# Performance work log

Hardware: AMD Instinct MI355X
Metric: run time of the kernel (lower is better)

## Reference

```python
import jax, jax.numpy as jnp
import numpy as np

HEADS = 16
DIM_HEAD = 64
QUERY_DIM = 1024
INNER = HEADS * DIM_HEAD


def setup_inputs() -> dict:
    key = jax.random.key(0)
    ks = jax.random.split(key, 6)
    b, n = 4, 2048
    s = 0.02
    return {
        "x": jax.random.normal(ks[0], (b, n, QUERY_DIM), dtype=jnp.float32),
        "Wq": jax.random.normal(ks[1], (QUERY_DIM, INNER), dtype=jnp.float32) * s,
        "Wk": jax.random.normal(ks[2], (QUERY_DIM, INNER), dtype=jnp.float32) * s,
        "Wv": jax.random.normal(ks[3], (QUERY_DIM, INNER), dtype=jnp.float32) * s,
        "Wo": jax.random.normal(ks[4], (INNER, QUERY_DIM), dtype=jnp.float32) * s,
        "bo": jax.random.normal(ks[5], (QUERY_DIM,), dtype=jnp.float32) * s,
    }


def reference(x, Wq, Wk, Wv, Wo, bo):
    b, n, _ = x.shape
    scale = DIM_HEAD ** (-0.5)
    # project and split heads: [b, n, inner] -> [b, h, n, d]
    def split(t):
        return t.reshape(b, n, HEADS, DIM_HEAD).transpose(0, 2, 1, 3)
    q = split(x @ Wq)
    k = split(x @ Wk)
    v = split(x @ Wv)
    sim = jnp.einsum('bhid,bhjd->bhij', q, k) * scale  # [b, h, n, n]
    attn = jax.nn.softmax(sim, axis=-1)
    out = jnp.einsum('bhij,bhjd->bhid', attn, v)  # [b, h, n, d]
    out = out.transpose(0, 2, 1, 3).reshape(b, n, INNER)
    return out @ Wo + bo
```

## Files before the change

### kernel.cpp

```cpp
#include <hip/hip_runtime.h>

typedef __attribute__((ext_vector_type(8))) short bf16x8;
typedef __attribute__((ext_vector_type(4))) float f32x4;
typedef __attribute__((ext_vector_type(16))) float f32x16;
typedef __attribute__((ext_vector_type(2))) unsigned u32x2;

__device__ __forceinline__ unsigned short f2b(float f) {
  union { float f; unsigned u; } x; x.f = f;
  unsigned r = x.u + 0x7fffu + ((x.u >> 16) & 1u);
  return (unsigned short)(r >> 16);
}

__device__ __forceinline__ int cvt_pk_bf16(float lo, float hi) {
  int r;
  asm("v_cvt_pk_bf16_f32 %0, %1, %2" : "=v"(r) : "v"(lo), "v"(hi));
  return r;
}

__device__ __forceinline__ float exp2_fast(float x) {
#if __has_builtin(__builtin_amdgcn_exp2f)
  return __builtin_amdgcn_exp2f(x);
#else
  return __expf(x * 0.69314718055994531f);
#endif
}

__device__ __forceinline__ void gl_lds16(const unsigned short* g, unsigned short* l) {
  __builtin_amdgcn_global_load_lds(
      (const __attribute__((address_space(1))) unsigned int*)(unsigned long long)g,
      (__attribute__((address_space(3))) unsigned int*)(unsigned)(unsigned long long)l,
      16, 0, 0);
}

#define MFMA(a, b, c) __builtin_amdgcn_mfma_f32_16x16x32_bf16((a), (b), (c), 0, 0, 0)
#define MFMA32(a, b, c) __builtin_amdgcn_mfma_f32_32x32x16_bf16((a), (b), (c), 0, 0, 0)

__global__ __launch_bounds__(256) void convert_x(const float* __restrict__ x,
                                                 unsigned short* __restrict__ xb) {
  int i = (blockIdx.x * 256 + threadIdx.x) * 4;
  float4 v = *(const float4*)(x + i);
  ushort4 o;
  o.x = f2b(v.x); o.y = f2b(v.y); o.z = f2b(v.z); o.w = f2b(v.w);
  *(ushort4*)(xb + i) = o;
}

__global__ __launch_bounds__(256) void transpose_w(const float* __restrict__ wq, const float* __restrict__ wk,
                                                   const float* __restrict__ wv, const float* __restrict__ wo,
                                                   unsigned short* __restrict__ tq, unsigned short* __restrict__ tk,
                                                   unsigned short* __restrict__ tv, unsigned short* __restrict__ to_) {
  int z = blockIdx.z;
  const float* W = (z == 0) ? wq : (z == 1) ? wk : (z == 2) ? wv : wo;
  unsigned short* T = (z == 0) ? tq : (z == 1) ? tk : (z == 2) ? tv : to_;
  float scale = (z == 0) ? 0.125f * 1.4426950408889634f : 1.0f;
  __shared__ float tile[64][65];
  int tr = blockIdx.y * 64, tc = blockIdx.x * 64;
  int t = threadIdx.x;
  int col = t & 63, r0 = (t >> 6) * 16;
#pragma unroll
  for (int r = 0; r < 16; r++)
    tile[r0 + r][col] = W[(long)(tr + r0 + r) * 1024 + tc + col];
  __syncthreads();
  int k = t & 63, n0 = (t >> 6) * 16;
#pragma unroll
  for (int n = 0; n < 16; n++)
    T[(long)(tc + n0 + n) * 1024 + tr + k] = f2b(tile[k][n0 + n] * scale);
}

__device__ __forceinline__ void gemm_tile_128(const unsigned short* __restrict__ A,
                                              const unsigned short* __restrict__ BT,
                                              int m0, int n0, f32x4 acc[4][4],
                                              unsigned short* As, unsigned short* Bs,
                                              int lane, int wid) {
  const int wr = wid >> 1, wc = wid & 1;
  const int c = lane & 15, g = lane >> 4;
  for (int kt = 0; kt < 32; kt++) {
    __syncthreads();
#pragma unroll
    for (int ii = 0; ii < 2; ii++) {
      int chunk = (wid * 2 + ii) * 64 + lane;
      int row = chunk >> 2, rc = chunk & 3;
      gl_lds16(A + (long)(m0 + row) * 1024 + kt * 32 + rc * 8, As + (wid * 2 + ii) * 512);
      gl_lds16(BT + (long)(n0 + row) * 1024 + kt * 32 + rc * 8, Bs + (wid * 2 + ii) * 512);
    }
    __syncthreads();
    bf16x8 af[4], bfr[4];
#pragma unroll
    for (int mi = 0; mi < 4; mi++)
      af[mi] = *(const bf16x8*)(As + (wr * 64 + mi * 16 + c) * 32 + g * 8);
#pragma unroll
    for (int ni = 0; ni < 4; ni++)
      bfr[ni] = *(const bf16x8*)(Bs + (wc * 64 + ni * 16 + c) * 32 + g * 8);
#pragma unroll
    for (int mi = 0; mi < 4; mi++)
#pragma unroll
      for (int ni = 0; ni < 4; ni++)
        acc[mi][ni] = MFMA(af[mi], bfr[ni], acc[mi][ni]);
  }
}

__global__ __launch_bounds__(256) void gemm_qkv(const unsigned short* __restrict__ xb,
                                                const unsigned short* __restrict__ wtq,
                                                const unsigned short* __restrict__ wtk,
                                                const unsigned short* __restrict__ wtv,
                                                unsigned short* __restrict__ Qw,
                                                unsigned short* __restrict__ Kw,
                                                unsigned short* __restrict__ Vtw) {
  __shared__ unsigned short As[128 * 32], Bs[128 * 32];
  int m0 = blockIdx.x * 128;
  int nglob = blockIdx.y * 128;
  int which = nglob >> 10;
  const unsigned short* BT = (which == 0) ? wtq : (which == 1) ? wtk : wtv;
  int n0 = nglob & 1023;
  int lane = threadIdx.x & 63, wid = threadIdx.x >> 6;
  f32x4 acc[4][4] = {};
  gemm_tile_128(xb, BT, m0, n0, acc, As, Bs, lane, wid);

  const int wr = wid >> 1, wc = wid & 1;
  const int c = lane & 15, g = lane >> 4;
  int b = m0 >> 11;
  int ibase = (m0 & 2047);
#pragma unroll
  for (int mi = 0; mi < 4; mi++) {
    int irow0 = ibase + wr * 64 + mi * 16 + g * 4;
#pragma unroll
    for (int ni = 0; ni < 4; ni++) {
      int nl = n0 + wc * 64 + ni * 16 + c;
      int h = nl >> 6, d = nl & 63;
      if (which == 2) {
        ushort4 pk;
        pk.x = f2b(acc[mi][ni][0]); pk.y = f2b(acc[mi][ni][1]);
        pk.z = f2b(acc[mi][ni][2]); pk.w = f2b(acc[mi][ni][3]);
        *(ushort4*)(Vtw + ((long)(b * 16 + h) * 64 + d) * 2048 + irow0) = pk;
      } else {
        unsigned short* dst = (which == 0) ? Qw : Kw;
#pragma unroll
        for (int r = 0; r < 4; r++)
          dst[((long)(b * 16 + h) * 2048 + irow0 + r) * 64 + d] = f2b(acc[mi][ni][r]);
      }
    }
  }
}

__global__ __launch_bounds__(512) void attn(const unsigned short* __restrict__ Qw,
                                            const unsigned short* __restrict__ Kw,
                                            const unsigned short* __restrict__ Vtw,
                                            unsigned short* __restrict__ Ow) {
  int ib = blockIdx.y * 8 + blockIdx.x;
  int xcd = ib & 7, j = ib >> 3;
  int bh = xcd * 8 + (j >> 3);
  int qt = j & 7;
  int t = threadIdx.x;
  int lane = t & 63, wid = t >> 6;
  int c5 = lane & 31, h = lane >> 5;
  __shared__ unsigned short Ks[2][64 * 64];
  __shared__ unsigned short Vs[2][64 * 64];

  const unsigned short* Qp = Qw + ((long)bh * 2048 + qt * 256 + wid * 32 + c5) * 64 + h * 8;
  bf16x8 qf[4];
#pragma unroll
  for (int dK = 0; dK < 4; dK++) qf[dK] = *(const bf16x8*)(Qp + dK * 16);

  f32x16 oacc0 = {}, oacc1 = {};
  float ls0 = 0.f, ls1 = 0.f, ls2 = 0.f, ls3 = 0.f;

  const unsigned short* Kbase = Kw + (long)bh * 2048 * 64;
  const unsigned short* Vbase = Vtw + (long)bh * 64 * 2048;

#define STAGE(jt_, buf_)                                                              \
  {                                                                                   \
    int row = t >> 3, ch = t & 7;                                                     \
    int sw = ch ^ (row & 7);                                                          \
    gl_lds16(Kbase + (long)((jt_) * 64 + row) * 64 + sw * 8, &Ks[buf_][t * 8]);       \
    gl_lds16(Vbase + (long)row * 2048 + (jt_) * 64 + sw * 8, &Vs[buf_][t * 8]);       \
  }

  STAGE(0, 0);

  union FR { int i[4]; bf16x8 v; };

  for (int jt = 0; jt < 32; jt++) {
    int buf = jt & 1;
    __syncthreads();
    if (jt + 1 < 32) STAGE(jt + 1, buf ^ 1);

    f32x16 s0 = {}, s1 = {};
#pragma unroll
    for (int dK = 0; dK < 4; dK++) {
      int sw = ((dK * 2 + h) ^ (c5 & 7)) * 8;
      bf16x8 k0 = *(const bf16x8*)(&Ks[buf][c5 * 64 + sw]);
      bf16x8 k1 = *(const bf16x8*)(&Ks[buf][c5 * 64 + sw + 2048]);
      s0 = MFMA32(k0, qf[dK], s0);
      s1 = MFMA32(k1, qf[dK], s1);
    }

    int pk[2][4][2];
#pragma unroll
    for (int q2 = 0; q2 < 4; q2++) {
      float a0 = exp2_fast(s0[q2 * 4 + 0]), a1 = exp2_fast(s0[q2 * 4 + 1]);
      float a2 = exp2_fast(s0[q2 * 4 + 2]), a3 = exp2_fast(s0[q2 * 4 + 3]);
      ls0 += a0 + a1; ls1 += a2 + a3;
      pk[0][q2][0] = cvt_pk_bf16(a0, a1);
      pk[0][q2][1] = cvt_pk_bf16(a2, a3);
      float b0 = exp2_fast(s1[q2 * 4 + 0]), b1 = exp2_fast(s1[q2 * 4 + 1]);
      float b2 = exp2_fast(s1[q2 * 4 + 2]), b3 = exp2_fast(s1[q2 * 4 + 3]);
      ls2 += b0 + b1; ls3 += b2 + b3;
      pk[1][q2][0] = cvt_pk_bf16(b0, b1);
      pk[1][q2][1] = cvt_pk_bf16(b2, b3);
    }

#pragma unroll
    for (int kblk = 0; kblk < 4; kblk++) {
      int kvb = kblk >> 1, e2c = (kblk & 1) * 2;
      u32x2 p0 = __builtin_amdgcn_permlane32_swap((unsigned)pk[kvb][e2c][0],
                                                  (unsigned)pk[kvb][e2c + 1][0], false, false);
      u32x2 p1 = __builtin_amdgcn_permlane32_swap((unsigned)pk[kvb][e2c][1],
                                                  (unsigned)pk[kvb][e2c + 1][1], false, false);
      FR fr;
      fr.i[0] = (int)p0[0];
      fr.i[1] = (int)p1[0];
      fr.i[2] = (int)p0[1];
      fr.i[3] = (int)p1[1];
      int sw = ((kblk * 2 + h) ^ (c5 & 7)) * 8;
      bf16x8 v0 = *(const bf16x8*)(&Vs[buf][c5 * 64 + sw]);
      bf16x8 v1 = *(const bf16x8*)(&Vs[buf][c5 * 64 + sw + 2048]);
      oacc0 = MFMA32(v0, fr.v, oacc0);
      oacc1 = MFMA32(v1, fr.v, oacc1);
    }
  }
#undef STAGE

  float lsum = ls0 + ls1 + ls2 + ls3;
  lsum += __shfl_xor(lsum, 32);
  float inv = 1.0f / lsum;
  int b = bh >> 4, hh = bh & 15;
  long row = (long)b * 2048 + qt * 256 + wid * 32 + c5;
  unsigned short* orow = Ow + row * 1024 + hh * 64;
#pragma unroll
  for (int dblk = 0; dblk < 2; dblk++) {
#pragma unroll
    for (int q2 = 0; q2 < 4; q2++) {
      float o0 = (dblk ? oacc1 : oacc0)[q2 * 4 + 0] * inv;
      float o1 = (dblk ? oacc1 : oacc0)[q2 * 4 + 1] * inv;
      float o2 = (dblk ? oacc1 : oacc0)[q2 * 4 + 2] * inv;
      float o3 = (dblk ? oacc1 : oacc0)[q2 * 4 + 3] * inv;
      ushort4 pkv;
      pkv.x = f2b(o0); pkv.y = f2b(o1); pkv.z = f2b(o2); pkv.w = f2b(o3);
      *(ushort4*)(orow + dblk * 32 + q2 * 8 + h * 4) = pkv;
    }
  }
}

__global__ __launch_bounds__(256) void gemm_out(const unsigned short* __restrict__ Ao,
                                                const unsigned short* __restrict__ wto,
                                                const float* __restrict__ bias,
                                                float* __restrict__ out) {
  __shared__ unsigned short As[128 * 32], Bs[128 * 32];
  int m0 = blockIdx.x * 128;
  int n0 = blockIdx.y * 128;
  int lane = threadIdx.x & 63, wid = threadIdx.x >> 6;
  f32x4 acc[4][4] = {};
  gemm_tile_128(Ao, wto, m0, n0, acc, As, Bs, lane, wid);
  const int wr = wid >> 1, wc = wid & 1;
  const int c = lane & 15, g = lane >> 4;
#pragma unroll
  for (int mi = 0; mi < 4; mi++)
#pragma unroll
    for (int ni = 0; ni < 4; ni++) {
      int col = n0 + wc * 64 + ni * 16 + c;
      float bv = bias[col];
#pragma unroll
      for (int r = 0; r < 4; r++) {
        int row = m0 + wr * 64 + mi * 16 + g * 4 + r;
        out[(long)row * 1024 + col] = acc[mi][ni][r] + bv;
      }
    }
}

extern "C" void kernel_launch(void* const* d_in, const int* in_sizes, int n_in,
                              void* d_out, int out_size, void* d_ws, size_t ws_size,
                              hipStream_t stream) {
  const float* x  = (const float*)d_in[0];
  const float* Wq = (const float*)d_in[1];
  const float* Wk = (const float*)d_in[2];
  const float* Wv = (const float*)d_in[3];
  const float* Wo = (const float*)d_in[4];
  const float* bo = (const float*)d_in[5];
  float* out = (float*)d_out;

  char* ws = (char*)d_ws;
  unsigned short* xb  = (unsigned short*)(ws);
  unsigned short* wtq = (unsigned short*)(ws + 16777216);
  unsigned short* wtk = (unsigned short*)(ws + 16777216 + 2097152);
  unsigned short* wtv = (unsigned short*)(ws + 16777216 + 2 * 2097152);
  unsigned short* wto = (unsigned short*)(ws + 16777216 + 3 * 2097152);
  unsigned short* Qw  = (unsigned short*)(ws + 25165824);
  unsigned short* Kw  = (unsigned short*)(ws + 25165824 + 16777216);
  unsigned short* Vtw = (unsigned short*)(ws + 25165824 + 2 * 16777216);
  unsigned short* Aow = xb;

  convert_x<<<8192, 256, 0, stream>>>(x, xb);
  transpose_w<<<dim3(16, 16, 4), 256, 0, stream>>>(Wq, Wk, Wv, Wo, wtq, wtk, wtv, wto);
  gemm_qkv<<<dim3(64, 24), 256, 0, stream>>>(xb, wtq, wtk, wtv, Qw, Kw, Vtw);
  attn<<<dim3(8, 64), 512, 0, stream>>>(Qw, Kw, Vtw, Aow);
  gemm_out<<<dim3(64, 8), 256, 0, stream>>>(Aow, wto, bo, out);
}
```

Measured before the change: 178.3 us.

## Double-buffer LDS tiles in projection GEMMs and remap blocks per XCD

The shared 128x128 GEMM tile loop now keeps two LDS buffers. It issues the global-to-LDS loads for the next K step before computing on the current one, so each iteration needs one barrier instead of two and load latency can overlap the MFMAs. Both GEMM kernels also remap the linear block index so that consecutive tiles land on the same XCD, which is meant to improve L2 reuse of the A and B panels. LDS use per block doubles, which may lower occupancy. Correctness relies on the barrier waiting for the outstanding async LDS loads.

```diff
diff --git a/kernel.cpp b/kernel.cpp
--- a/kernel.cpp
+++ b/kernel.cpp
@@ -66,6 +66,20 @@
     T[(long)(tc + n0 + n) * 1024 + tr + k] = f2b(tile[k][n0 + n] * scale);
 }
 
+__device__ __forceinline__ void gemm_stage128(const unsigned short* __restrict__ A,
+                                              const unsigned short* __restrict__ BT,
+                                              int m0, int n0, int kt,
+                                              unsigned short* As, unsigned short* Bs,
+                                              int lane, int wid) {
+#pragma unroll
+  for (int ii = 0; ii < 2; ii++) {
+    int chunk = (wid * 2 + ii) * 64 + lane;
+    int row = chunk >> 2, rc = chunk & 3;
+    gl_lds16(A + (long)(m0 + row) * 1024 + kt * 32 + rc * 8, As + (wid * 2 + ii) * 512);
+    gl_lds16(BT + (long)(n0 + row) * 1024 + kt * 32 + rc * 8, Bs + (wid * 2 + ii) * 512);
+  }
+}
+
 __device__ __forceinline__ void gemm_tile_128(const unsigned short* __restrict__ A,
                                               const unsigned short* __restrict__ BT,
                                               int m0, int n0, f32x4 acc[4][4],
@@ -73,23 +87,21 @@
                                               int lane, int wid) {
   const int wr = wid >> 1, wc = wid & 1;
   const int c = lane & 15, g = lane >> 4;
+  gemm_stage128(A, BT, m0, n0, 0, As, Bs, lane, wid);
   for (int kt = 0; kt < 32; kt++) {
+    int buf = kt & 1;
+    const unsigned short* Ab = As + buf * 4096;
+    const unsigned short* Bb = Bs + buf * 4096;
     __syncthreads();
-#pragma unroll
-    for (int ii = 0; ii < 2; ii++) {
-      int chunk = (wid * 2 + ii) * 64 + lane;
-      int row = chunk >> 2, rc = chunk & 3;
-      gl_lds16(A + (long)(m0 + row) * 1024 + kt * 32 + rc * 8, As + (wid * 2 + ii) * 512);
-      gl_lds16(BT + (long)(n0 + row) * 1024 + kt * 32 + rc * 8, Bs + (wid * 2 + ii) * 512);
-    }
-    __syncthreads();
+    if (kt + 1 < 32)
+      gemm_stage128(A, BT, m0, n0, kt + 1, As + (buf ^ 1) * 4096, Bs + (buf ^ 1) * 4096, lane, wid);
     bf16x8 af[4], bfr[4];
 #pragma unroll
     for (int mi = 0; mi < 4; mi++)
-      af[mi] = *(const bf16x8*)(As + (wr * 64 + mi * 16 + c) * 32 + g * 8);
+      af[mi] = *(const bf16x8*)(Ab + (wr * 64 + mi * 16 + c) * 32 + g * 8);
 #pragma unroll
     for (int ni = 0; ni < 4; ni++)
-      bfr[ni] = *(const bf16x8*)(Bs + (wc * 64 + ni * 16 + c) * 32 + g * 8);
+      bfr[ni] = *(const bf16x8*)(Bb + (wc * 64 + ni * 16 + c) * 32 + g * 8);
 #pragma unroll
     for (int mi = 0; mi < 4; mi++)
 #pragma unroll
@@ -105,9 +117,12 @@
                                                 unsigned short* __restrict__ Qw,
                                                 unsigned short* __restrict__ Kw,
                                                 unsigned short* __restrict__ Vtw) {
-  __shared__ unsigned short As[128 * 32], Bs[128 * 32];
-  int m0 = blockIdx.x * 128;
-  int nglob = blockIdx.y * 128;
+  __shared__ unsigned short As[2 * 128 * 32], Bs[2 * 128 * 32];
+  int lin = blockIdx.y * 64 + blockIdx.x;
+  int work = (lin & 7) * 192 + (lin >> 3);
+  int mb = work / 24, nb = work % 24;
+  int m0 = mb * 128;
+  int nglob = nb * 128;
   int which = nglob >> 10;
   const unsigned short* BT = (which == 0) ? wtq : (which == 1) ? wtk : wtv;
   int n0 = nglob & 1023;
@@ -254,9 +269,12 @@
                                                 const unsigned short* __restrict__ wto,
                                                 const float* __restrict__ bias,
                                                 float* __restrict__ out) {
-  __shared__ unsigned short As[128 * 32], Bs[128 * 32];
-  int m0 = blockIdx.x * 128;
-  int n0 = blockIdx.y * 128;
+  __shared__ unsigned short As[2 * 128 * 32], Bs[2 * 128 * 32];
+  int lin = blockIdx.y * 64 + blockIdx.x;
+  int work = (lin & 7) * 64 + (lin >> 3);
+  int mb = work / 8, nb = work % 8;
+  int m0 = mb * 128;
+  int n0 = nb * 128;
   int lane = threadIdx.x & 63, wid = threadIdx.x >> 6;
   f32x4 acc[4][4] = {};
   gemm_tile_128(Ao, wto, m0, n0, acc, As, Bs, lane, wid);
```

Result: slower. 188.3 us (+5.6%).

## Triple-buffer GEMM LDS tiles with async prefetch and XOR swizzle

Applied to the files above, without the earlier changes.

Restructures the shared GEMM mainloop used by the QKV and output projections into a three-stage LDS ring. Global-to-LDS loads run two k-tiles ahead, and a vmcnt wait plus a single barrier per iteration replaces the two barriers that serialized loads and MFMAs. It also XOR-swizzles the 16-byte chunk placement within each LDS row to reduce bank conflicts on fragment reads. This triples GEMM LDS usage, which may lower occupancy, and it relies on hand-counted vmcnt values being correct.

```diff
diff --git a/kernel.cpp b/kernel.cpp
--- a/kernel.cpp
+++ b/kernel.cpp
@@ -66,6 +66,21 @@
     T[(long)(tc + n0 + n) * 1024 + tr + k] = f2b(tile[k][n0 + n] * scale);
 }
 
+__device__ __forceinline__ void gemm_stage128(const unsigned short* __restrict__ A,
+                                              const unsigned short* __restrict__ BT,
+                                              int m0, int n0, int kt,
+                                              unsigned short* As, unsigned short* Bs,
+                                              int lane, int wid) {
+#pragma unroll
+  for (int ii = 0; ii < 2; ii++) {
+    int chunk = (wid * 2 + ii) * 64 + lane;
+    int row = chunk >> 2, rc = chunk & 3;
+    int rcs = rc ^ ((row >> 1) & 3);
+    gl_lds16(A + (long)(m0 + row) * 1024 + kt * 32 + rcs * 8, As + (wid * 2 + ii) * 512);
+    gl_lds16(BT + (long)(n0 + row) * 1024 + kt * 32 + rcs * 8, Bs + (wid * 2 + ii) * 512);
+  }
+}
+
 __device__ __forceinline__ void gemm_tile_128(const unsigned short* __restrict__ A,
                                               const unsigned short* __restrict__ BT,
                                               int m0, int n0, f32x4 acc[4][4],
@@ -73,23 +88,33 @@
                                               int lane, int wid) {
   const int wr = wid >> 1, wc = wid & 1;
   const int c = lane & 15, g = lane >> 4;
+  gemm_stage128(A, BT, m0, n0, 0, As, Bs, lane, wid);
+  gemm_stage128(A, BT, m0, n0, 1, As + 4096, Bs + 4096, lane, wid);
   for (int kt = 0; kt < 32; kt++) {
-    __syncthreads();
-#pragma unroll
-    for (int ii = 0; ii < 2; ii++) {
-      int chunk = (wid * 2 + ii) * 64 + lane;
-      int row = chunk >> 2, rc = chunk & 3;
-      gl_lds16(A + (long)(m0 + row) * 1024 + kt * 32 + rc * 8, As + (wid * 2 + ii) * 512);
-      gl_lds16(BT + (long)(n0 + row) * 1024 + kt * 32 + rc * 8, Bs + (wid * 2 + ii) * 512);
-    }
-    __syncthreads();
+    int buf = kt % 3;
+    const unsigned short* Ab = As + buf * 4096;
+    const unsigned short* Bb = Bs + buf * 4096;
+    if (kt < 31)
+      asm volatile("s_waitcnt vmcnt(4)" ::: "memory");
+    else
+      asm volatile("s_waitcnt vmcnt(0)" ::: "memory");
+    __builtin_amdgcn_s_barrier();
+    __builtin_amdgcn_sched_barrier(0);
+    if (kt + 2 < 32) {
+      int nb = (kt + 2) % 3;
+      gemm_stage128(A, BT, m0, n0, kt + 2, As + nb * 4096, Bs + nb * 4096, lane, wid);
+    }
     bf16x8 af[4], bfr[4];
 #pragma unroll
-    for (int mi = 0; mi < 4; mi++)
-      af[mi] = *(const bf16x8*)(As + (wr * 64 + mi * 16 + c) * 32 + g * 8);
-#pragma unroll
-    for (int ni = 0; ni < 4; ni++)
-      bfr[ni] = *(const bf16x8*)(Bs + (wc * 64 + ni * 16 + c) * 32 + g * 8);
+    for (int mi = 0; mi < 4; mi++) {
+      int row = wr * 64 + mi * 16 + c;
+      af[mi] = *(const bf16x8*)(Ab + row * 32 + (g ^ ((row >> 1) & 3)) * 8);
+    }
+#pragma unroll
+    for (int ni = 0; ni < 4; ni++) {
+      int row = wc * 64 + ni * 16 + c;
+      bfr[ni] = *(const bf16x8*)(Bb + row * 32 + (g ^ ((row >> 1) & 3)) * 8);
+    }
 #pragma unroll
     for (int mi = 0; mi < 4; mi++)
 #pragma unroll
@@ -105,7 +130,7 @@
                                                 unsigned short* __restrict__ Qw,
                                                 unsigned short* __restrict__ Kw,
                                                 unsigned short* __restrict__ Vtw) {
-  __shared__ unsigned short As[128 * 32], Bs[128 * 32];
+  __shared__ unsigned short As[3 * 128 * 32], Bs[3 * 128 * 32];
   int m0 = blockIdx.x * 128;
   int nglob = blockIdx.y * 128;
   int which = nglob >> 10;
@@ -254,7 +279,7 @@
                                                 const unsigned short* __restrict__ wto,
                                                 const float* __restrict__ bias,
                                                 float* __restrict__ out) {
-  __shared__ unsigned short As[128 * 32], Bs[128 * 32];
+  __shared__ unsigned short As[3 * 128 * 32], Bs[3 * 128 * 32];
   int m0 = blockIdx.x * 128;
   int n0 = blockIdx.y * 128;
   int lane = threadIdx.x & 63, wid = threadIdx.x >> 6;
```

New measurement: 180.7 us. No clear change (+1.3%).

## Rewrite projection GEMMs as 256x256 double-buffered tiles with swizzled LDS

Applied to the files above, without the earlier changes.

Replaces the 128x128, single-buffered, K=32 GEMM core with a 256x256 tile over 512 threads, K=64 per step and double-buffered LDS. The next tile's loads are split across four phases and overlapped with MFMA work, using s_setprio around the math. An XOR swizzle on LDS columns is meant to avoid bank conflicts. This cuts the grid size: gemm_out drops to 128 blocks and gemm_qkv to 384, which may underfill the 256 CUs and raises per-block register and LDS pressure (128KB LDS).

```diff
diff --git a/kernel.cpp b/kernel.cpp
--- a/kernel.cpp
+++ b/kernel.cpp
@@ -66,62 +66,104 @@
     T[(long)(tc + n0 + n) * 1024 + tr + k] = f2b(tile[k][n0 + n] * scale);
 }
 
-__device__ __forceinline__ void gemm_tile_128(const unsigned short* __restrict__ A,
+__device__ __forceinline__ void gemm_core_256(const unsigned short* __restrict__ A,
                                               const unsigned short* __restrict__ BT,
-                                              int m0, int n0, f32x4 acc[4][4],
+                                              int m0, int n0,
                                               unsigned short* As, unsigned short* Bs,
-                                              int lane, int wid) {
-  const int wr = wid >> 1, wc = wid & 1;
+                                              f32x4 acc[8][4]) {
+  const int t = threadIdx.x;
+  const int lane = t & 63;
+  const int wid = t >> 6;
+  const int wr = wid >> 2, wc = wid & 3;
   const int c = lane & 15, g = lane >> 4;
-  for (int kt = 0; kt < 32; kt++) {
-    __syncthreads();
-#pragma unroll
-    for (int ii = 0; ii < 2; ii++) {
-      int chunk = (wid * 2 + ii) * 64 + lane;
-      int row = chunk >> 2, rc = chunk & 3;
-      gl_lds16(A + (long)(m0 + row) * 1024 + kt * 32 + rc * 8, As + (wid * 2 + ii) * 512);
-      gl_lds16(BT + (long)(n0 + row) * 1024 + kt * 32 + rc * 8, Bs + (wid * 2 + ii) * 512);
-    }
-    __syncthreads();
-    bf16x8 af[4], bfr[4];
-#pragma unroll
-    for (int mi = 0; mi < 4; mi++)
-      af[mi] = *(const bf16x8*)(As + (wr * 64 + mi * 16 + c) * 32 + g * 8);
-#pragma unroll
-    for (int ni = 0; ni < 4; ni++)
-      bfr[ni] = *(const bf16x8*)(Bs + (wc * 64 + ni * 16 + c) * 32 + g * 8);
-#pragma unroll
-    for (int mi = 0; mi < 4; mi++)
-#pragma unroll
-      for (int ni = 0; ni < 4; ni++)
-        acc[mi][ni] = MFMA(af[mi], bfr[ni], acc[mi][ni]);
-  }
-}
-
-__global__ __launch_bounds__(256) void gemm_qkv(const unsigned short* __restrict__ xb,
+
+#define STAGE_HALF(MAT, base, kt_, dst, hh)                                           \
+  {                                                                                   \
+    _Pragma("unroll")                                                                 \
+    for (int j = 0; j < 2; j++) {                                                     \
+      int idx = j * 512 + t;                                                          \
+      int srow = idx >> 3, pc = idx & 7;                                              \
+      int sc = pc ^ (srow & 7);                                                       \
+      gl_lds16(MAT + (long)((base) + (hh) * 128 + srow) * 1024 + (kt_) * 64 + sc * 8, \
+               (dst) + (hh) * 8192 + idx * 8);                                        \
+    }                                                                                 \
+  }
+
+  STAGE_HALF(A, m0, 0, As, 0);
+  STAGE_HALF(A, m0, 0, As, 1);
+  STAGE_HALF(BT, n0, 0, Bs, 0);
+  STAGE_HALF(BT, n0, 0, Bs, 1);
+
+  for (int kt = 0; kt < 16; kt++) {
+    unsigned short* Ab = As + (kt & 1) * 16384;
+    unsigned short* Bb = Bs + (kt & 1) * 16384;
+    unsigned short* An = As + ((kt & 1) ^ 1) * 16384;
+    unsigned short* Bn = Bs + ((kt & 1) ^ 1) * 16384;
+    asm volatile("s_waitcnt vmcnt(0)" ::: "memory");
+    __builtin_amdgcn_s_barrier();
+
+    bf16x8 bfr[2][4];
+#pragma unroll
+    for (int ph = 0; ph < 4; ph++) {
+      const int qm = ph & 1, ks = ph >> 1;
+      bf16x8 af[4];
+      if (qm == 0) {
+#pragma unroll
+        for (int ni = 0; ni < 4; ni++) {
+          int row = wc * 64 + ni * 16 + c;
+          bfr[ks][ni] = *(const bf16x8*)(Bb + row * 64 + ((ks * 4 + g) ^ (row & 7)) * 8);
+        }
+      }
+#pragma unroll
+      for (int i = 0; i < 4; i++) {
+        int row = wr * 128 + (qm * 4 + i) * 16 + c;
+        af[i] = *(const bf16x8*)(Ab + row * 64 + ((ks * 4 + g) ^ (row & 7)) * 8);
+      }
+      if (kt + 1 < 16) {
+        if (ph == 0) STAGE_HALF(A, m0, kt + 1, An, 0)
+        else if (ph == 1) STAGE_HALF(A, m0, kt + 1, An, 1)
+        else if (ph == 2) STAGE_HALF(BT, n0, kt + 1, Bn, 0)
+        else STAGE_HALF(BT, n0, kt + 1, Bn, 1)
+      }
+      __builtin_amdgcn_s_barrier();
+      __builtin_amdgcn_s_setprio(1);
+#pragma unroll
+      for (int i = 0; i < 4; i++)
+#pragma unroll
+        for (int ni = 0; ni < 4; ni++)
+          acc[qm * 4 + i][ni] = MFMA(af[i], bfr[ks][ni], acc[qm * 4 + i][ni]);
+      __builtin_amdgcn_s_setprio(0);
+      __builtin_amdgcn_s_barrier();
+    }
+  }
+#undef STAGE_HALF
+}
+
+__global__ __launch_bounds__(512) void gemm_qkv(const unsigned short* __restrict__ xb,
                                                 const unsigned short* __restrict__ wtq,
                                                 const unsigned short* __restrict__ wtk,
                                                 const unsigned short* __restrict__ wtv,
                                                 unsigned short* __restrict__ Qw,
                                                 unsigned short* __restrict__ Kw,
                                                 unsigned short* __restrict__ Vtw) {
-  __shared__ unsigned short As[128 * 32], Bs[128 * 32];
-  int m0 = blockIdx.x * 128;
-  int nglob = blockIdx.y * 128;
-  int which = nglob >> 10;
+  __shared__ unsigned short As[2 * 16384], Bs[2 * 16384];
+  int m0 = blockIdx.x * 256;
+  int nglob0 = blockIdx.y * 256;
+  int which = nglob0 >> 10;
   const unsigned short* BT = (which == 0) ? wtq : (which == 1) ? wtk : wtv;
-  int n0 = nglob & 1023;
-  int lane = threadIdx.x & 63, wid = threadIdx.x >> 6;
-  f32x4 acc[4][4] = {};
-  gemm_tile_128(xb, BT, m0, n0, acc, As, Bs, lane, wid);
-
-  const int wr = wid >> 1, wc = wid & 1;
+  int n0 = nglob0 & 1023;
+  f32x4 acc[8][4] = {};
+  gemm_core_256(xb, BT, m0, n0, As, Bs, acc);
+
+  const int t = threadIdx.x;
+  const int lane = t & 63, wid = t >> 6;
+  const int wr = wid >> 2, wc = wid & 3;
   const int c = lane & 15, g = lane >> 4;
   int b = m0 >> 11;
-  int ibase = (m0 & 2047);
-#pragma unroll
-  for (int mi = 0; mi < 4; mi++) {
-    int irow0 = ibase + wr * 64 + mi * 16 + g * 4;
+  int ibase = m0 & 2047;
+#pragma unroll
+  for (int mi = 0; mi < 8; mi++) {
+    int irow0 = ibase + wr * 128 + mi * 16 + g * 4;
 #pragma unroll
     for (int ni = 0; ni < 4; ni++) {
       int nl = n0 + wc * 64 + ni * 16 + c;
@@ -139,6 +181,34 @@
       }
     }
   }
+}
+
+__global__ __launch_bounds__(512) void gemm_out(const unsigned short* __restrict__ Ao,
+                                                const unsigned short* __restrict__ wto,
+                                                const float* __restrict__ bias,
+                                                float* __restrict__ out) {
+  __shared__ unsigned short As[2 * 16384], Bs[2 * 16384];
+  int m0 = blockIdx.x * 256;
+  int n0 = blockIdx.y * 256;
+  f32x4 acc[8][4] = {};
+  gemm_core_256(Ao, wto, m0, n0, As, Bs, acc);
+
+  const int t = threadIdx.x;
+  const int lane = t & 63, wid = t >> 6;
+  const int wr = wid >> 2, wc = wid & 3;
+  const int c = lane & 15, g = lane >> 4;
+#pragma unroll
+  for (int mi = 0; mi < 8; mi++)
+#pragma unroll
+    for (int ni = 0; ni < 4; ni++) {
+      int col = n0 + wc * 64 + ni * 16 + c;
+      float bv = bias[col];
+#pragma unroll
+      for (int r = 0; r < 4; r++) {
+        int row = m0 + wr * 128 + mi * 16 + g * 4 + r;
+        out[(long)row * 1024 + col] = acc[mi][ni][r] + bv;
+      }
+    }
 }
 
 __global__ __launch_bounds__(512) void attn(const unsigned short* __restrict__ Qw,
@@ -250,32 +320,6 @@
   }
 }
 
-__global__ __launch_bounds__(256) void gemm_out(const unsigned short* __restrict__ Ao,
-                                                const unsigned short* __restrict__ wto,
-                                                const float* __restrict__ bias,
-                                                float* __restrict__ out) {
-  __shared__ unsigned short As[128 * 32], Bs[128 * 32];
-  int m0 = blockIdx.x * 128;
-  int n0 = blockIdx.y * 128;
-  int lane = threadIdx.x & 63, wid = threadIdx.x >> 6;
-  f32x4 acc[4][4] = {};
-  gemm_tile_128(Ao, wto, m0, n0, acc, As, Bs, lane, wid);
-  const int wr = wid >> 1, wc = wid & 1;
-  const int c = lane & 15, g = lane >> 4;
-#pragma unroll
-  for (int mi = 0; mi < 4; mi++)
-#pragma unroll
-    for (int ni = 0; ni < 4; ni++) {
-      int col = n0 + wc * 64 + ni * 16 + c;
-      float bv = bias[col];
-#pragma unroll
-      for (int r = 0; r < 4; r++) {
-        int row = m0 + wr * 64 + mi * 16 + g * 4 + r;
-        out[(long)row * 1024 + col] = acc[mi][ni][r] + bv;
-      }
-    }
-}
-
 extern "C" void kernel_launch(void* const* d_in, const int* in_sizes, int n_in,
                               void* d_out, int out_size, void* d_ws, size_t ws_size,
                               hipStream_t stream) {
@@ -300,7 +344,7 @@
 
   convert_x<<<8192, 256, 0, stream>>>(x, xb);
   transpose_w<<<dim3(16, 16, 4), 256, 0, stream>>>(Wq, Wk, Wv, Wo, wtq, wtk, wtv, wto);
-  gemm_qkv<<<dim3(64, 24), 256, 0, stream>>>(xb, wtq, wtk, wtv, Qw, Kw, Vtw);
+  gemm_qkv<<<dim3(32, 12), 512, 0, stream>>>(xb, wtq, wtk, wtv, Qw, Kw, Vtw);
   attn<<<dim3(8, 64), 512, 0, stream>>>(Qw, Kw, Vtw, Aow);
-  gemm_out<<<dim3(64, 8), 256, 0, stream>>>(Aow, wto, bo, out);
-}
+  gemm_out<<<dim3(32, 4), 512, 0, stream>>>(Aow, wto, bo, out);
+}
```

New measurement: 184.5 us. 1.03x slower.
